# Kernel tuning notes

Measured on AMD Instinct MI355X. Metric: run time of the kernel, lower is better.

The kernel has to match this reference:

```python
import jax, jax.numpy as jnp
import numpy as np

WINDOW = 16  # hardcoded in module __init__

B, S, E, H = 2, 2048, 1024, 16
HD = E // H


def setup_inputs() -> dict:
    key = jax.random.key(0)
    k1, k2, k3, k4, k5, k6 = jax.random.split(key, 6)
    input_embeddings = jax.random.normal(k1, (B, S, E), dtype=jnp.float32)
    token_ids = jax.random.randint(k2, (B, S), 0, 32000, dtype=jnp.int64)
    # nn.MultiheadAttention parameters: packed in_proj (3E, E) + bias, out_proj (E, E) + bias
    in_proj_weight = jax.random.normal(k3, (3 * E, E), dtype=jnp.float32) * 0.02
    in_proj_bias = jax.random.normal(k4, (3 * E,), dtype=jnp.float32) * 0.02
    out_proj_weight = jax.random.normal(k5, (E, E), dtype=jnp.float32) * 0.02
    out_proj_bias = jax.random.normal(k6, (E,), dtype=jnp.float32) * 0.02
    return {
        "input_embeddings": input_embeddings,
        "token_ids": token_ids,
        "in_proj_weight": in_proj_weight,
        "in_proj_bias": in_proj_bias,
        "out_proj_weight": out_proj_weight,
        "out_proj_bias": out_proj_bias,
    }


def _blocked_mask(seq_len: int) -> jnp.ndarray:
    # Module sets mask[i, j] = True for j in [i - WINDOW, i] (17 positions).
    # PyTorch bool attn_mask: True = NOT allowed to attend.
    i = jnp.arange(seq_len)[:, None]
    j = jnp.arange(seq_len)[None, :]
    return (j <= i) & (j >= i - WINDOW)  # [S, S] bool, True = masked out


def reference(input_embeddings, token_ids, in_proj_weight, in_proj_bias,
              out_proj_weight, out_proj_bias):
    x = input_embeddings  # [B, S, E]
    b, s, e = x.shape
    # Packed QKV projection (torch Linear: y = x W^T + b)
    qkv = jnp.einsum('bse,fe->bsf', x, in_proj_weight) + in_proj_bias  # [B, S, 3E]
    q, k, v = jnp.split(qkv, 3, axis=-1)
    # Split heads: [B, H, S, HD]
    q = q.reshape(b, s, H, HD).transpose(0, 2, 1, 3)
    k = k.reshape(b, s, H, HD).transpose(0, 2, 1, 3)
    v = v.reshape(b, s, H, HD).transpose(0, 2, 1, 3)
    scale = 1.0 / jnp.sqrt(jnp.asarray(HD, dtype=x.dtype))
    scores = jnp.einsum('bhqd,bhkd->bhqk', q * scale, k)  # [B, H, S, S]
    blocked = _blocked_mask(s)  # True = masked
    scores = jnp.where(blocked[None, None, :, :], -jnp.inf, scores)
    attn = jax.nn.softmax(scores, axis=-1)
    ctx = jnp.einsum('bhqk,bhkd->bhqd', attn, v)  # [B, H, S, HD]
    ctx = ctx.transpose(0, 2, 1, 3).reshape(b, s, e)
    out = jnp.einsum('bse,fe->bsf', ctx, out_proj_weight) + out_proj_bias
    return out
```

## Files before the change

kernel.cpp:

```cpp
#include <hip/hip_runtime.h>

typedef __attribute__((ext_vector_type(8))) __bf16 bf16x8;
typedef __attribute__((ext_vector_type(4))) float f32x4;
typedef unsigned short u16;
typedef unsigned int u32;

#define MFMA16(a, b, c) __builtin_amdgcn_mfma_f32_16x16x32_bf16((a), (b), (c), 0, 0, 0)

__device__ __forceinline__ u16 f2bf(float f) {
  return (u16)((__float_as_uint(f) + 0x8000u) >> 16);
}

#define BDIM 2
#define SDIM 2048
#define EDIM 1024
#define HDIM 16
#define HD 64
#define MDIM (BDIM * SDIM)

#define SC_C1 0.1803368801111355f

typedef __attribute__((address_space(3))) void lds_void;
typedef __attribute__((address_space(1))) void g_void;

__device__ __forceinline__ void async_lds16(const void* g, void* lds_byte) {
  __builtin_amdgcn_global_load_lds((const g_void*)g, (lds_void*)lds_byte, 16, 0, 0);
}

__global__ __launch_bounds__(256) void cvt3_kernel(
    const float* __restrict__ s0, u16* __restrict__ d0, int n0,
    const float* __restrict__ s1, u16* __restrict__ d1, int n1,
    const float* __restrict__ s2, u16* __restrict__ d2, int n2) {
  int i = (blockIdx.x * 256 + threadIdx.x) * 8;
  const float* s;
  u16* d;
  if (i < n0) {
    s = s0 + i; d = d0 + i;
  } else if (i < n0 + n1) {
    s = s1 + (i - n0); d = d1 + (i - n0);
  } else if (i < n0 + n1 + n2) {
    s = s2 + (i - n0 - n1); d = d2 + (i - n0 - n1);
  } else {
    return;
  }
  float4 f0 = *(const float4*)(s);
  float4 f1 = *(const float4*)(s + 4);
  union { uint4 u; u16 h[8]; } o;
  o.h[0] = f2bf(f0.x); o.h[1] = f2bf(f0.y); o.h[2] = f2bf(f0.z); o.h[3] = f2bf(f0.w);
  o.h[4] = f2bf(f1.x); o.h[5] = f2bf(f1.y); o.h[6] = f2bf(f1.z); o.h[7] = f2bf(f1.w);
  *(uint4*)(d) = o.u;
}

__global__ __launch_bounds__(256) void gemm_qkv_kernel(
    const u16* __restrict__ X, const u16* __restrict__ W,
    const float* __restrict__ bias, u16* __restrict__ qb,
    u16* __restrict__ kb, u16* __restrict__ vtb) {
  __shared__ __align__(16) u16 As[128 * 64];
  __shared__ __align__(16) u16 Bs[128 * 64];
  const int m0 = blockIdx.x * 128, n0 = blockIdx.y * 128;
  const bool isV = (n0 >= 2 * EDIM);
  const int t = threadIdx.x;
  const int l = t & 63;
  const int quad = l >> 4, col = l & 15;
  const int wid = t >> 6;
  const int mh = wid & 1, nh = wid >> 1;
  const int wofs = (t & 192) << 4;
  f32x4 acc[4][4] = {};
  const u16* Ab = X + (size_t)m0 * EDIM;
  const u16* Bb = W + (size_t)n0 * EDIM;
  char* AsB = (char*)As;
  char* BsB = (char*)Bs;

  for (int k0 = 0; k0 < EDIM; k0 += 64) {
    __syncthreads();
#pragma unroll
    for (int p = 0; p < 4; p++) {
      int idx = p * 256 + t;
      int row = idx >> 3;
      int gch = (idx & 7) ^ (row & 7);
      async_lds16(Ab + (size_t)row * EDIM + k0 + gch * 8, AsB + p * 4096 + wofs);
      async_lds16(Bb + (size_t)row * EDIM + k0 + gch * 8, BsB + p * 4096 + wofs);
    }
    __syncthreads();
#pragma unroll
    for (int kk = 0; kk < 2; kk++) {
      bf16x8 af[4], bfr[4];
#pragma unroll
      for (int i = 0; i < 4; i++) {
        int ra = 64 * mh + 16 * i + col;
        af[i] = *(const bf16x8*)&As[ra * 64 + (((kk * 4 + quad) ^ (ra & 7)) * 8)];
        int rb = 64 * nh + 16 * i + col;
        bfr[i] = *(const bf16x8*)&Bs[rb * 64 + (((kk * 4 + quad) ^ (rb & 7)) * 8)];
      }
      if (isV) {
#pragma unroll
        for (int i = 0; i < 4; i++)
#pragma unroll
          for (int j = 0; j < 4; j++)
            acc[i][j] = MFMA16(bfr[i], af[j], acc[i][j]);
      } else {
#pragma unroll
        for (int i = 0; i < 4; i++)
#pragma unroll
          for (int j = 0; j < 4; j++)
            acc[i][j] = MFMA16(af[i], bfr[j], acc[i][j]);
      }
    }
  }

  if (isV) {
#pragma unroll
    for (int i = 0; i < 4; i++)
#pragma unroll
      for (int j = 0; j < 4; j++)
#pragma unroll
        for (int r = 0; r < 4; r++) {
          int n = n0 + 64 * nh + 16 * i + quad * 4 + r;
          int m = m0 + 64 * mh + 16 * j + col;
          float val = acc[i][j][r] + bias[n];
          int e = n & 1023;
          int hh = e >> 6, d = e & 63;
          int bb = m >> 11, s = m & 2047;
          vtb[(((size_t)(bb * HDIM + hh)) * HD + d) * SDIM + s] = f2bf(val);
        }
  } else {
    const float qscale = (n0 < EDIM) ? SC_C1 : 1.0f;
#pragma unroll
    for (int i = 0; i < 4; i++)
#pragma unroll
      for (int j = 0; j < 4; j++)
#pragma unroll
        for (int r = 0; r < 4; r++) {
          int m = m0 + 64 * mh + 16 * i + quad * 4 + r;
          int n = n0 + 64 * nh + 16 * j + col;
          float val = (acc[i][j][r] + bias[n]) * qscale;
          int which = n >> 10, e = n & 1023;
          int hh = e >> 6, d = e & 63;
          int bb = m >> 11, s = m & 2047;
          u16* dst = (which == 0) ? qb : kb;
          dst[(((size_t)(bb * HDIM + hh)) * SDIM + s) * HD + d] = f2bf(val);
        }
  }
}

__global__ __launch_bounds__(256) void attn_kernel(
    const u16* __restrict__ qg, const u16* __restrict__ kg,
    const u16* __restrict__ vtg, u16* __restrict__ ctx) {
  __shared__ __align__(16) u16 KB[2][64 * 64];
  __shared__ __align__(16) u16 VB[2][64 * 64];
  __shared__ __align__(16) u16 Ps[64 * 64];

  const int bh = blockIdx.x;
  const int q0 = blockIdx.y * 64;
  const int t = threadIdx.x;
  const int wid = t >> 6, l = t & 63;
  const int quad = l >> 4, col = l & 15;
  const size_t base = (size_t)bh * SDIM * HD;

  bf16x8 aq[2];
  {
    const u16* qp = qg + base + (size_t)(q0 + 16 * wid + col) * HD + quad * 8;
    aq[0] = *(const bf16x8*)(qp);
    aq[1] = *(const bf16x8*)(qp + 32);
  }
  const int qi = q0 + 16 * wid + col;
  const int qrow = q0 + 16 * wid + quad * 4;

  const int srow = t >> 3;
  const int g = (t & 7) ^ (srow & 7);
  const u16* kptr = kg + base + (size_t)srow * HD + g * 8;
  const u16* vptr = vtg + base + (size_t)srow * SDIM + g * 8;
  const int wofs = (t & 192) << 4;

  auto stageK = [&](int kt, int buf) {
    char* d = (char*)KB[buf] + wofs;
    async_lds16(kptr + (size_t)(kt * 64) * HD, d);
    async_lds16(kptr + (size_t)(kt * 64 + 32) * HD, d + 4096);
  };
  auto stageV = [&](int kt, int buf) {
    char* d = (char*)VB[buf] + wofs;
    async_lds16(vptr + kt * 64, d);
    async_lds16(vptr + (size_t)32 * SDIM + kt * 64, d + 4096);
  };

  auto qkt = [&](const u16* Kt, f32x4* sco) {
#pragma unroll
    for (int half = 0; half < 2; half++)
#pragma unroll
      for (int ct = 0; ct < 4; ct++) {
        int r = 16 * ct + col;
        int phys = (4 * half + quad) ^ (r & 7);
        bf16x8 kf = *(const bf16x8*)&Kt[r * 64 + phys * 8];
        sco[ct] = MFMA16(kf, aq[half], sco[ct]);
      }
  };

  char* PsB = (char*)Ps;
  const int prow = 16 * wid + col;
  int wPs[4], rPs[2];
#pragma unroll
  for (int ct = 0; ct < 4; ct++)
    wPs[ct] = prow * 128 + (((2 * ct + (quad >> 1)) ^ (col & 7)) * 16) +
              (quad & 1) * 8;
#pragma unroll
  for (int half = 0; half < 2; half++)
    rPs[half] = prow * 128 + (((half * 4 + quad) ^ (col & 7)) * 16);

  float psum = 0.f;
  f32x4 oacc[4] = {};
  f32x4 scA[4] = {}, scB[4];

  auto smax = [&](int kt, f32x4 (&cur)[4], bool band) {
#pragma unroll
    for (int ct = 0; ct < 4; ct++) {
      float p[4];
#pragma unroll
      for (int r = 0; r < 4; r++) {
        float s = cur[ct][r];
        if (band) {
          int j = kt * 64 + 16 * ct + quad * 4 + r;
          if (j <= qi && j + 16 >= qi) s = -1.0e30f;
        }
        p[r] = __builtin_exp2f(s);
        psum += p[r];
      }
      u32 w0, w1;
      asm("v_cvt_pk_bf16_f32 %0, %1, %2" : "=v"(w0) : "v"(p[0]), "v"(p[1]));
      asm("v_cvt_pk_bf16_f32 %0, %1, %2" : "=v"(w1) : "v"(p[2]), "v"(p[3]));
      uint2 w;
      w.x = w0;
      w.y = w1;
      *(uint2*)(PsB + wPs[ct]) = w;
    }
  };

  auto pv = [&](const u16* Vt) {
#pragma unroll
    for (int half = 0; half < 2; half++) {
      bf16x8 pa = *(const bf16x8*)(PsB + rPs[half]);
#pragma unroll
      for (int dt = 0; dt < 4; dt++) {
        int vr = 16 * dt + col;
        int phys = (4 * half + quad) ^ (vr & 7);
        bf16x8 vf = *(const bf16x8*)&Vt[vr * 64 + phys * 8];
        oacc[dt] = MFMA16(pa, vf, oacc[dt]);
      }
    }
  };

  const int NT = SDIM / 64;

  auto body = [&](int kt, f32x4 (&cur)[4], f32x4 (&nxt)[4]) {
    __syncthreads();
    if (kt + 2 < NT) stageK(kt + 2, kt & 1);
    if (kt + 1 < NT) {
      stageV(kt + 1, (kt + 1) & 1);
#pragma unroll
      for (int ct = 0; ct < 4; ct++) nxt[ct] = f32x4{0.f, 0.f, 0.f, 0.f};
      qkt(KB[(kt + 1) & 1], nxt);
    }
    bool band = (kt * 64 <= q0 + 63) && (kt * 64 + 63 >= q0 - 16);
    smax(kt, cur, band);
    pv(VB[kt & 1]);
  };

  stageK(0, 0);
  stageV(0, 0);
  __syncthreads();
  qkt(KB[0], scA);
  stageK(1, 1);

#pragma unroll 1
  for (int kt = 0; kt < NT; kt += 2) {
    body(kt, scA, scB);
    body(kt + 1, scB, scA);
  }

  psum += __shfl_xor(psum, 16, 64);
  psum += __shfl_xor(psum, 32, 64);

  const int b = bh >> 4, h = bh & 15;
  float linv[4];
#pragma unroll
  for (int r = 0; r < 4; r++)
    linv[r] = 1.0f / __shfl(psum, quad * 4 + r, 64);
#pragma unroll
  for (int dt = 0; dt < 4; dt++)
#pragma unroll
    for (int r = 0; r < 4; r++) {
      int qgl = qrow + r;
      int d = 16 * dt + col;
      ctx[((size_t)(b * SDIM + qgl)) * EDIM + h * HD + d] =
          f2bf(oacc[dt][r] * linv[r]);
    }
}

__global__ __launch_bounds__(256) void gemm_out_kernel(
    const u16* __restrict__ A, const u16* __restrict__ W,
    const float* __restrict__ bias, float* __restrict__ out) {
  __shared__ __align__(16) u16 As[128 * 64];
  __shared__ __align__(16) u16 Bs[128 * 64];
  const int m0 = blockIdx.x * 128, n0 = blockIdx.y * 128;
  const int t = threadIdx.x;
  const int l = t & 63;
  const int quad = l >> 4, col = l & 15;
  const int wid = t >> 6;
  const int mh = wid & 1, nh = wid >> 1;
  const int wofs = (t & 192) << 4;
  f32x4 acc[4][4] = {};
  const u16* Ab = A + (size_t)m0 * EDIM;
  const u16* Bb = W + (size_t)n0 * EDIM;
  char* AsB = (char*)As;
  char* BsB = (char*)Bs;

  for (int k0 = 0; k0 < EDIM; k0 += 64) {
    __syncthreads();
#pragma unroll
    for (int p = 0; p < 4; p++) {
      int idx = p * 256 + t;
      int row = idx >> 3;
      int gch = (idx & 7) ^ (row & 7);
      async_lds16(Ab + (size_t)row * EDIM + k0 + gch * 8, AsB + p * 4096 + wofs);
      async_lds16(Bb + (size_t)row * EDIM + k0 + gch * 8, BsB + p * 4096 + wofs);
    }
    __syncthreads();
#pragma unroll
    for (int kk = 0; kk < 2; kk++) {
      bf16x8 af[4], bfr[4];
#pragma unroll
      for (int i = 0; i < 4; i++) {
        int ra = 64 * mh + 16 * i + col;
        af[i] = *(const bf16x8*)&As[ra * 64 + (((kk * 4 + quad) ^ (ra & 7)) * 8)];
        int rb = 64 * nh + 16 * i + col;
        bfr[i] = *(const bf16x8*)&Bs[rb * 64 + (((kk * 4 + quad) ^ (rb & 7)) * 8)];
      }
#pragma unroll
      for (int i = 0; i < 4; i++)
#pragma unroll
        for (int j = 0; j < 4; j++)
          acc[i][j] = MFMA16(af[i], bfr[j], acc[i][j]);
    }
  }

#pragma unroll
  for (int i = 0; i < 4; i++)
#pragma unroll
    for (int j = 0; j < 4; j++)
#pragma unroll
      for (int r = 0; r < 4; r++) {
        int m = m0 + 64 * mh + 16 * i + quad * 4 + r;
        int n = n0 + 64 * nh + 16 * j + col;
        out[(size_t)m * EDIM + n] = acc[i][j][r] + bias[n];
      }
}

extern "C" void kernel_launch(void* const* d_in, const int* in_sizes, int n_in,
                              void* d_out, int out_size, void* d_ws,
                              size_t ws_size, hipStream_t stream) {
  const float* x = (const float*)d_in[0];
  const float* in_w = (const float*)d_in[2];
  const float* in_b = (const float*)d_in[3];
  const float* out_w = (const float*)d_in[4];
  const float* out_b = (const float*)d_in[5];
  float* out = (float*)d_out;

  char* ws = (char*)d_ws;
  u16* Xb  = (u16*)ws;
  u16* ctx = (u16*)ws;
  u16* qb  = (u16*)(ws + (size_t)( 8 << 20));
  u16* kb  = (u16*)(ws + (size_t)(16 << 20));
  u16* vtb = (u16*)(ws + (size_t)(24 << 20));
  u16* Wib = (u16*)(ws + (size_t)(32 << 20));
  u16* Wob = (u16*)(ws + (size_t)(38 << 20));

  const int nX = MDIM * EDIM;
  const int nWi = 3 * EDIM * EDIM;
  const int nWo = EDIM * EDIM;
  cvt3_kernel<<<(nX + nWi + nWo) / 8 / 256, 256, 0, stream>>>(
      x, Xb, nX, in_w, Wib, nWi, out_w, Wob, nWo);

  gemm_qkv_kernel<<<dim3(MDIM / 128, 3 * EDIM / 128), 256, 0, stream>>>(
      Xb, Wib, in_b, qb, kb, vtb);
  attn_kernel<<<dim3(BDIM * HDIM, SDIM / 64), 256, 0, stream>>>(qb, kb, vtb, ctx);
  gemm_out_kernel<<<dim3(MDIM / 128, EDIM / 128), 256, 0, stream>>>(
      ctx, Wob, out_b, out);
}
```

Baseline: 221.0 us.

## Triple-buffer K/V tiles with explicit vmcnt waits and MFMA priority hints

Measured after the change: 236.1 us. +6.9%, slower.

```diff
diff --git a/kernel.cpp b/kernel.cpp
--- a/kernel.cpp
+++ b/kernel.cpp
@@ -146,8 +146,8 @@
 __global__ __launch_bounds__(256) void attn_kernel(
     const u16* __restrict__ qg, const u16* __restrict__ kg,
     const u16* __restrict__ vtg, u16* __restrict__ ctx) {
-  __shared__ __align__(16) u16 KB[2][64 * 64];
-  __shared__ __align__(16) u16 VB[2][64 * 64];
+  __shared__ __align__(16) u16 KB[3][64 * 64];
+  __shared__ __align__(16) u16 VB[3][64 * 64];
   __shared__ __align__(16) u16 Ps[64 * 64];
 
   const int bh = blockIdx.x;
@@ -157,12 +157,14 @@
   const int quad = l >> 4, col = l & 15;
   const size_t base = (size_t)bh * SDIM * HD;
 
-  bf16x8 aq[2];
+  bf16x8 aq0, aq1;
   {
     const u16* qp = qg + base + (size_t)(q0 + 16 * wid + col) * HD + quad * 8;
-    aq[0] = *(const bf16x8*)(qp);
-    aq[1] = *(const bf16x8*)(qp + 32);
-  }
+    aq0 = *(const bf16x8*)(qp);
+    aq1 = *(const bf16x8*)(qp + 32);
+  }
+  asm volatile("" : "+v"(aq0), "+v"(aq1));
+
   const int qi = q0 + 16 * wid + col;
   const int qrow = q0 + 16 * wid + quad * 4;
 
@@ -185,30 +187,35 @@
 
   auto qkt = [&](const u16* Kt, f32x4* sco) {
 #pragma unroll
-    for (int half = 0; half < 2; half++)
+    for (int half = 0; half < 2; half++) {
+      bf16x8 aqh = half ? aq1 : aq0;
 #pragma unroll
       for (int ct = 0; ct < 4; ct++) {
         int r = 16 * ct + col;
         int phys = (4 * half + quad) ^ (r & 7);
         bf16x8 kf = *(const bf16x8*)&Kt[r * 64 + phys * 8];
-        sco[ct] = MFMA16(kf, aq[half], sco[ct]);
-      }
+        sco[ct] = MFMA16(kf, aqh, sco[ct]);
+      }
+    }
   };
 
   char* PsB = (char*)Ps;
   const int prow = 16 * wid + col;
-  int wPs[4], rPs[2];
+  const int sub0 = (col >> 3) << 3;
+  int wPs[4], rLo[2], rHi[2];
 #pragma unroll
   for (int ct = 0; ct < 4; ct++)
-    wPs[ct] = prow * 128 + (((2 * ct + (quad >> 1)) ^ (col & 7)) * 16) +
-              (quad & 1) * 8;
-#pragma unroll
-  for (int half = 0; half < 2; half++)
-    rPs[half] = prow * 128 + (((half * 4 + quad) ^ (col & 7)) * 16);
+    wPs[ct] = prow * 128 + (((2 * ct + (quad >> 1)) ^ (col & 7)) << 4) +
+              (((quad & 1) << 3) ^ sub0);
+#pragma unroll
+  for (int half = 0; half < 2; half++) {
+    int cb = prow * 128 + (((4 * half + quad) ^ (col & 7)) << 4);
+    rLo[half] = cb + sub0;
+    rHi[half] = cb + (8 - sub0);
+  }
 
   float psum = 0.f;
   f32x4 oacc[4] = {};
-  f32x4 scA[4] = {}, scB[4];
 
   auto smax = [&](int kt, f32x4 (&cur)[4], bool band) {
 #pragma unroll
@@ -237,7 +244,11 @@
   auto pv = [&](const u16* Vt) {
 #pragma unroll
     for (int half = 0; half < 2; half++) {
-      bf16x8 pa = *(const bf16x8*)(PsB + rPs[half]);
+      uint2 lo = *(const uint2*)(PsB + rLo[half]);
+      uint2 hi = *(const uint2*)(PsB + rHi[half]);
+      uint4 pw;
+      pw.x = lo.x; pw.y = lo.y; pw.z = hi.x; pw.w = hi.y;
+      bf16x8 pa = __builtin_bit_cast(bf16x8, pw);
 #pragma unroll
       for (int dt = 0; dt < 4; dt++) {
         int vr = 16 * dt + col;
@@ -250,30 +261,35 @@
 
   const int NT = SDIM / 64;
 
-  auto body = [&](int kt, f32x4 (&cur)[4], f32x4 (&nxt)[4]) {
-    __syncthreads();
-    if (kt + 2 < NT) stageK(kt + 2, kt & 1);
-    if (kt + 1 < NT) {
-      stageV(kt + 1, (kt + 1) & 1);
-#pragma unroll
-      for (int ct = 0; ct < 4; ct++) nxt[ct] = f32x4{0.f, 0.f, 0.f, 0.f};
-      qkt(KB[(kt + 1) & 1], nxt);
-    }
-    bool band = (kt * 64 <= q0 + 63) && (kt * 64 + 63 >= q0 - 16);
-    smax(kt, cur, band);
-    pv(VB[kt & 1]);
-  };
-
   stageK(0, 0);
   stageV(0, 0);
-  __syncthreads();
-  qkt(KB[0], scA);
   stageK(1, 1);
-
+  stageV(1, 1);
+
+  int cur = 0, stg = 2;
 #pragma unroll 1
-  for (int kt = 0; kt < NT; kt += 2) {
-    body(kt, scA, scB);
-    body(kt + 1, scB, scA);
+  for (int kt = 0; kt < NT; ++kt) {
+    if (kt < NT - 1) {
+      asm volatile("s_waitcnt vmcnt(4)" ::: "memory");
+    } else {
+      asm volatile("s_waitcnt vmcnt(0)" ::: "memory");
+    }
+    __builtin_amdgcn_s_barrier();
+    if (kt + 2 < NT) {
+      stageK(kt + 2, stg);
+      stageV(kt + 2, stg);
+    }
+    f32x4 sc[4] = {};
+    __builtin_amdgcn_s_setprio(1);
+    qkt(KB[cur], sc);
+    __builtin_amdgcn_s_setprio(0);
+    bool band = (kt * 64 <= q0 + 63) && (kt * 64 + 63 >= q0 - 16);
+    smax(kt, sc, band);
+    __builtin_amdgcn_s_setprio(1);
+    pv(VB[cur]);
+    __builtin_amdgcn_s_setprio(0);
+    cur = (cur == 2) ? 0 : cur + 1;
+    stg = (stg == 2) ? 0 : stg + 1;
   }
 
   psum += __shfl_xor(psum, 16, 64);
```

## Rewrite attention with 32x32 MFMA tiles, register-resident P and triple-buffered V

Applied to the files above, without the earlier changes.

Measured after the change: 219.7 us. About the same (-0.6%).

```diff
diff --git a/kernel.cpp b/kernel.cpp
--- a/kernel.cpp
+++ b/kernel.cpp
@@ -2,10 +2,12 @@
 
 typedef __attribute__((ext_vector_type(8))) __bf16 bf16x8;
 typedef __attribute__((ext_vector_type(4))) float f32x4;
+typedef __attribute__((ext_vector_type(16))) float f32x16;
 typedef unsigned short u16;
 typedef unsigned int u32;
 
 #define MFMA16(a, b, c) __builtin_amdgcn_mfma_f32_16x16x32_bf16((a), (b), (c), 0, 0, 0)
+#define MFMA32(a, b, c) __builtin_amdgcn_mfma_f32_32x32x16_bf16((a), (b), (c), 0, 0, 0)
 
 __device__ __forceinline__ u16 f2bf(float f) {
   return (u16)((__float_as_uint(f) + 0x8000u) >> 16);
@@ -147,24 +149,25 @@
     const u16* __restrict__ qg, const u16* __restrict__ kg,
     const u16* __restrict__ vtg, u16* __restrict__ ctx) {
   __shared__ __align__(16) u16 KB[2][64 * 64];
-  __shared__ __align__(16) u16 VB[2][64 * 64];
-  __shared__ __align__(16) u16 Ps[64 * 64];
+  __shared__ __align__(16) u16 VB[3][64 * 64];
 
   const int bh = blockIdx.x;
-  const int q0 = blockIdx.y * 64;
+  const int q0 = blockIdx.y * 128;
   const int t = threadIdx.x;
   const int wid = t >> 6, l = t & 63;
-  const int quad = l >> 4, col = l & 15;
+  const int col = l & 31, half = l >> 5;
   const size_t base = (size_t)bh * SDIM * HD;
 
-  bf16x8 aq[2];
+  const int qw0 = q0 + 32 * wid;
+  const int qi = qw0 + col;
+
+  bf16x8 bq[4];
   {
-    const u16* qp = qg + base + (size_t)(q0 + 16 * wid + col) * HD + quad * 8;
-    aq[0] = *(const bf16x8*)(qp);
-    aq[1] = *(const bf16x8*)(qp + 32);
-  }
-  const int qi = q0 + 16 * wid + col;
-  const int qrow = q0 + 16 * wid + quad * 4;
+    const u16* qp = qg + base + (size_t)qi * HD + half * 8;
+#pragma unroll
+    for (int f = 0; f < 4; f++) bq[f] = *(const bf16x8*)(qp + f * 16);
+  }
+  asm volatile("" : "+v"(bq[0]), "+v"(bq[1]), "+v"(bq[2]), "+v"(bq[3]));
 
   const int srow = t >> 3;
   const int g = (t & 7) ^ (srow & 7);
@@ -183,92 +186,99 @@
     async_lds16(vptr + (size_t)32 * SDIM + kt * 64, d + 4096);
   };
 
-  auto qkt = [&](const u16* Kt, f32x4* sco) {
-#pragma unroll
-    for (int half = 0; half < 2; half++)
-#pragma unroll
-      for (int ct = 0; ct < 4; ct++) {
-        int r = 16 * ct + col;
-        int phys = (4 * half + quad) ^ (r & 7);
-        bf16x8 kf = *(const bf16x8*)&Kt[r * 64 + phys * 8];
-        sco[ct] = MFMA16(kf, aq[half], sco[ct]);
-      }
-  };
-
-  char* PsB = (char*)Ps;
-  const int prow = 16 * wid + col;
-  int wPs[4], rPs[2];
-#pragma unroll
-  for (int ct = 0; ct < 4; ct++)
-    wPs[ct] = prow * 128 + (((2 * ct + (quad >> 1)) ^ (col & 7)) * 16) +
-              (quad & 1) * 8;
-#pragma unroll
-  for (int half = 0; half < 2; half++)
-    rPs[half] = prow * 128 + (((half * 4 + quad) ^ (col & 7)) * 16);
-
-  float psum = 0.f;
-  f32x4 oacc[4] = {};
-  f32x4 scA[4] = {}, scB[4];
-
-  auto smax = [&](int kt, f32x4 (&cur)[4], bool band) {
-#pragma unroll
-    for (int ct = 0; ct < 4; ct++) {
-      float p[4];
-#pragma unroll
-      for (int r = 0; r < 4; r++) {
-        float s = cur[ct][r];
+  auto qkt = [&](const u16* Kt, f32x16 (&sco)[2]) {
+#pragma unroll
+    for (int s = 0; s < 2; s++)
+#pragma unroll
+      for (int f = 0; f < 4; f++) {
+        int kr = 32 * s + col;
+        int phys = (2 * f + half) ^ (kr & 7);
+        bf16x8 kf = *(const bf16x8*)&Kt[kr * 64 + phys * 8];
+        sco[s] = MFMA32(kf, bq[f], sco[s]);
+      }
+  };
+
+  float ps0 = 0.f, ps1 = 0.f, ps2 = 0.f, ps3 = 0.f;
+  f32x16 oacc[2] = {};
+
+  auto smax = [&](int kt, f32x16 (&cur)[2], bool band, u32 (&w)[2][8]) {
+#pragma unroll
+    for (int s = 0; s < 2; s++) {
+      float p[16];
+#pragma unroll
+      for (int r = 0; r < 16; r++) {
+        float v = cur[s][r];
         if (band) {
-          int j = kt * 64 + 16 * ct + quad * 4 + r;
-          if (j <= qi && j + 16 >= qi) s = -1.0e30f;
+          int j = kt * 64 + 32 * s + (r & 3) + 8 * (r >> 2) + 4 * half;
+          if (j <= qi && j + 16 >= qi) v = -1.0e30f;
         }
-        p[r] = __builtin_exp2f(s);
-        psum += p[r];
-      }
-      u32 w0, w1;
-      asm("v_cvt_pk_bf16_f32 %0, %1, %2" : "=v"(w0) : "v"(p[0]), "v"(p[1]));
-      asm("v_cvt_pk_bf16_f32 %0, %1, %2" : "=v"(w1) : "v"(p[2]), "v"(p[3]));
-      uint2 w;
-      w.x = w0;
-      w.y = w1;
-      *(uint2*)(PsB + wPs[ct]) = w;
-    }
-  };
-
-  auto pv = [&](const u16* Vt) {
-#pragma unroll
-    for (int half = 0; half < 2; half++) {
-      bf16x8 pa = *(const bf16x8*)(PsB + rPs[half]);
-#pragma unroll
-      for (int dt = 0; dt < 4; dt++) {
-        int vr = 16 * dt + col;
-        int phys = (4 * half + quad) ^ (vr & 7);
-        bf16x8 vf = *(const bf16x8*)&Vt[vr * 64 + phys * 8];
-        oacc[dt] = MFMA16(pa, vf, oacc[dt]);
-      }
-    }
+        p[r] = __builtin_exp2f(v);
+      }
+#pragma unroll
+      for (int r = 0; r < 16; r++) {
+        if ((r & 3) == 0) ps0 += p[r];
+        else if ((r & 3) == 1) ps1 += p[r];
+        else if ((r & 3) == 2) ps2 += p[r];
+        else ps3 += p[r];
+      }
+#pragma unroll
+      for (int j = 0; j < 8; j++) {
+        u32 wv;
+        asm("v_cvt_pk_bf16_f32 %0, %1, %2" : "=v"(wv) : "v"(p[2 * j]), "v"(p[2 * j + 1]));
+        w[s][j] = wv;
+      }
+    }
+  };
+
+  auto pv = [&](const u16* Vt, u32 (&w)[2][8]) {
+#pragma unroll
+    for (int s = 0; s < 2; s++)
+#pragma unroll
+      for (int b2 = 0; b2 < 2; b2++) {
+        u32 x0 = w[s][4 * b2 + 0], x1 = w[s][4 * b2 + 1];
+        u32 y0 = w[s][4 * b2 + 2], y1 = w[s][4 * b2 + 3];
+        asm("v_permlane32_swap_b32 %0, %1" : "+v"(x0), "+v"(y0));
+        asm("v_permlane32_swap_b32 %0, %1" : "+v"(x1), "+v"(y1));
+        uint4 pw;
+        pw.x = x0; pw.y = x1; pw.z = y0; pw.w = y1;
+        bf16x8 pa = __builtin_bit_cast(bf16x8, pw);
+        int ks = 2 * s + b2;
+#pragma unroll
+        for (int dt = 0; dt < 2; dt++) {
+          int vr = 32 * dt + col;
+          int phys = (2 * ks + half) ^ (vr & 7);
+          bf16x8 vf = *(const bf16x8*)&Vt[vr * 64 + phys * 8];
+          oacc[dt] = MFMA32(vf, pa, oacc[dt]);
+        }
+      }
   };
 
   const int NT = SDIM / 64;
 
-  auto body = [&](int kt, f32x4 (&cur)[4], f32x4 (&nxt)[4]) {
-    __syncthreads();
-    if (kt + 2 < NT) stageK(kt + 2, kt & 1);
+  auto body = [&](int kt, f32x16 (&cur)[2], f32x16 (&nxt)[2]) {
+    __syncthreads();
     if (kt + 1 < NT) {
-      stageV(kt + 1, (kt + 1) & 1);
-#pragma unroll
-      for (int ct = 0; ct < 4; ct++) nxt[ct] = f32x4{0.f, 0.f, 0.f, 0.f};
+      nxt[0] = (f32x16){};
+      nxt[1] = (f32x16){};
       qkt(KB[(kt + 1) & 1], nxt);
     }
-    bool band = (kt * 64 <= q0 + 63) && (kt * 64 + 63 >= q0 - 16);
-    smax(kt, cur, band);
-    pv(VB[kt & 1]);
-  };
-
+    if (kt + 2 < NT) {
+      stageK(kt + 2, kt & 1);
+      stageV(kt + 2, (unsigned)(kt + 2) % 3u);
+    }
+    u32 w[2][8];
+    bool band = (kt * 64 <= qw0 + 31) && (kt * 64 + 63 >= qw0 - 16);
+    smax(kt, cur, band, w);
+    pv(VB[(unsigned)kt % 3u], w);
+  };
+
+  f32x16 scA[2] = {}, scB[2] = {};
   stageK(0, 0);
   stageV(0, 0);
   __syncthreads();
   qkt(KB[0], scA);
   stageK(1, 1);
+  stageV(1, 1);
 
 #pragma unroll 1
   for (int kt = 0; kt < NT; kt += 2) {
@@ -276,22 +286,24 @@
     body(kt + 1, scB, scA);
   }
 
-  psum += __shfl_xor(psum, 16, 64);
+  float psum = (ps0 + ps1) + (ps2 + ps3);
   psum += __shfl_xor(psum, 32, 64);
+  float linv = 1.0f / psum;
 
   const int b = bh >> 4, h = bh & 15;
-  float linv[4];
-#pragma unroll
-  for (int r = 0; r < 4; r++)
-    linv[r] = 1.0f / __shfl(psum, quad * 4 + r, 64);
-#pragma unroll
-  for (int dt = 0; dt < 4; dt++)
-#pragma unroll
-    for (int r = 0; r < 4; r++) {
-      int qgl = qrow + r;
-      int d = 16 * dt + col;
-      ctx[((size_t)(b * SDIM + qgl)) * EDIM + h * HD + d] =
-          f2bf(oacc[dt][r] * linv[r]);
+  u16* cbase = ctx + ((size_t)(b * SDIM + qi)) * EDIM + h * HD;
+#pragma unroll
+  for (int dt = 0; dt < 2; dt++)
+#pragma unroll
+    for (int a = 0; a < 4; a++) {
+      float v0 = oacc[dt][4 * a + 0] * linv, v1 = oacc[dt][4 * a + 1] * linv;
+      float v2 = oacc[dt][4 * a + 2] * linv, v3 = oacc[dt][4 * a + 3] * linv;
+      u32 w0, w1;
+      asm("v_cvt_pk_bf16_f32 %0, %1, %2" : "=v"(w0) : "v"(v0), "v"(v1));
+      asm("v_cvt_pk_bf16_f32 %0, %1, %2" : "=v"(w1) : "v"(v2), "v"(v3));
+      uint2 st;
+      st.x = w0; st.y = w1;
+      *(uint2*)(cbase + 32 * dt + 8 * a + 4 * half) = st;
     }
 }
 
@@ -381,7 +393,7 @@
 
   gemm_qkv_kernel<<<dim3(MDIM / 128, 3 * EDIM / 128), 256, 0, stream>>>(
       Xb, Wib, in_b, qb, kb, vtb);
-  attn_kernel<<<dim3(BDIM * HDIM, SDIM / 64), 256, 0, stream>>>(qb, kb, vtb, ctx);
+  attn_kernel<<<dim3(BDIM * HDIM, SDIM / 128), 256, 0, stream>>>(qb, kb, vtb, ctx);
   gemm_out_kernel<<<dim3(MDIM / 128, EDIM / 128), 256, 0, stream>>>(
       ctx, Wob, out_b, out);
 }
```
